# Kernel optimization log

Measured on AMD Instinct MI355X. Metric: run time of the kernel, lower is better.

Reference implementation:

```python
import jax, jax.numpy as jnp
import numpy as np

B = 16384      # batch size
L = 50         # max bag length (padded jagged)
V0, D0 = 1_000_000, 64
V1, D1 = 100_000, 128


def setup_inputs() -> dict:
    key = jax.random.key(0)
    k0, k1, k2, k3, k4, k5 = jax.random.split(key, 6)
    indices0 = jax.random.randint(k0, (B, L), 0, V0, dtype=jnp.int32)
    lengths0 = jax.random.randint(k1, (B,), 0, L + 1, dtype=jnp.int32)
    indices1 = jax.random.randint(k2, (B, L), 0, V1, dtype=jnp.int32)
    lengths1 = jax.random.randint(k3, (B,), 0, L + 1, dtype=jnp.int32)
    E0 = jax.random.normal(k4, (V0, D0), dtype=jnp.float32) * 0.01
    E1 = jax.random.normal(k5, (V1, D1), dtype=jnp.float32) * 0.01
    return {"indices0": indices0, "lengths0": lengths0,
            "indices1": indices1, "lengths1": lengths1,
            "E0": E0, "E1": E1}


def _bag_sum(E, idx, lens):
    # E: [V, D], idx: [B, L] padded indices, lens: [B] valid counts.
    # Gather rows then masked SUM-pool over the (jagged) bag dim.
    rows = E[idx]                                      # [B, L, D]
    mask = (jnp.arange(idx.shape[1])[None, :] < lens[:, None]).astype(E.dtype)  # [B, L]
    return jnp.einsum('bld,bl->bd', rows, mask)        # [B, D]


def reference(indices0, lengths0, indices1, lengths1, E0, E1):
    # EmbeddingBagCollection: per-table pooled lookup, concat along feature dim
    # (KeyedTensor layout: [B, D0 + D1]).
    p0 = _bag_sum(E0, indices0, lengths0)  # [B, 64]
    p1 = _bag_sum(E1, indices1, lengths1)  # [B, 128]
    return jnp.concatenate([p0, p1], axis=1)
```

## Files before the change

kernel.cpp:

```cpp
#include <hip/hip_runtime.h>


#define BB 16384
#define LL 50
#define D0 64
#define D1 128
#define DOUT 192

__global__ __launch_bounds__(256) void embbag_kernel(
    const int* __restrict__ idx0, const int* __restrict__ len0,
    const int* __restrict__ idx1, const int* __restrict__ len1,
    const float* __restrict__ E0, const float* __restrict__ E1,
    float* __restrict__ out)
{
    const int t    = threadIdx.x;
    const int wid  = t >> 6;
    const int lane = t & 63;
    const int b = blockIdx.x * 2 + (wid >> 1);
    const int table = wid & 1;
    if (b >= BB) return;

    if (table == 0) {
        const int sub = lane >> 4;
        const int j   = lane & 15;
        const int n   = len0[b];
        const int* __restrict__ ip = idx0 + b * LL;
        float4 acc = make_float4(0.f, 0.f, 0.f, 0.f);
        for (int base = 0; base < n; base += 4) {
            const int row = base + sub;
            if (row < n) {
                const int id = ip[row];
                const float4 v = *reinterpret_cast<const float4*>(
                    E0 + (size_t)id * D0 + j * 4);
                acc.x += v.x; acc.y += v.y; acc.z += v.z; acc.w += v.w;
            }
        }
        #pragma unroll
        for (int m = 16; m < 64; m <<= 1) {
            acc.x += __shfl_xor(acc.x, m, 64);
            acc.y += __shfl_xor(acc.y, m, 64);
            acc.z += __shfl_xor(acc.z, m, 64);
            acc.w += __shfl_xor(acc.w, m, 64);
        }
        if (sub == 0) {
            *reinterpret_cast<float4*>(out + (size_t)b * DOUT + j * 4) = acc;
        }
    } else {
        const int sub = lane >> 5;
        const int j   = lane & 31;
        const int n   = len1[b];
        const int* __restrict__ ip = idx1 + b * LL;
        float4 acc = make_float4(0.f, 0.f, 0.f, 0.f);
        for (int base = 0; base < n; base += 2) {
            const int row = base + sub;
            if (row < n) {
                const int id = ip[row];
                const float4 v = *reinterpret_cast<const float4*>(
                    E1 + (size_t)id * D1 + j * 4);
                acc.x += v.x; acc.y += v.y; acc.z += v.z; acc.w += v.w;
            }
        }
        acc.x += __shfl_xor(acc.x, 32, 64);
        acc.y += __shfl_xor(acc.y, 32, 64);
        acc.z += __shfl_xor(acc.z, 32, 64);
        acc.w += __shfl_xor(acc.w, 32, 64);
        if (sub == 0) {
            *reinterpret_cast<float4*>(out + (size_t)b * DOUT + D0 + j * 4) = acc;
        }
    }
}

extern "C" void kernel_launch(void* const* d_in, const int* in_sizes, int n_in,
                              void* d_out, int out_size, void* d_ws, size_t ws_size,
                              hipStream_t stream) {
    const int*   idx0 = (const int*)d_in[0];
    const int*   len0 = (const int*)d_in[1];
    const int*   idx1 = (const int*)d_in[2];
    const int*   len1 = (const int*)d_in[3];
    const float* E0   = (const float*)d_in[4];
    const float* E1   = (const float*)d_in[5];
    float* out = (float*)d_out;

    const int grid = BB / 2;
    embbag_kernel<<<grid, 256, 0, stream>>>(idx0, len0, idx1, len1, E0, E1, out);
}
```

Measured before the change: 60.81 us.

## Preload bag indices per wave and fully unroll gathers with masked clamped loads

Each wave now loads all 50 bag indices with one coalesced read and distributes them with shuffles, removing the dependent index load before every row gather. The loop is fully unrolled to a fixed trip count, with out-of-range rows clamped to a valid row and multiplied by zero. This lets many independent row loads be in flight at once, and two accumulators split the add chain. Empty bags exit early after writing zeros. The trade-off is redundant row reads, since padded rows fetch the last valid row again (mostly cache hits), and more registers, capped by the added occupancy hint in launch bounds.

Result: faster. 51.46 us (-15.4%).

```diff
diff --git a/kernel.cpp b/kernel.cpp
--- a/kernel.cpp
+++ b/kernel.cpp
@@ -7,7 +7,7 @@
 #define D1 128
 #define DOUT 192
 
-__global__ __launch_bounds__(256) void embbag_kernel(
+__global__ __launch_bounds__(256, 4) void embbag_kernel(
     const int* __restrict__ idx0, const int* __restrict__ len0,
     const int* __restrict__ idx1, const int* __restrict__ len1,
     const float* __restrict__ E0, const float* __restrict__ E1,
@@ -18,54 +18,83 @@
     const int lane = t & 63;
     const int b = blockIdx.x * 2 + (wid >> 1);
     const int table = wid & 1;
-    if (b >= BB) return;
 
     if (table == 0) {
+        const int n   = len0[b];
         const int sub = lane >> 4;
         const int j   = lane & 15;
-        const int n   = len0[b];
+        float* op = out + (size_t)b * DOUT + j * 4;
+        if (n == 0) {
+            if (sub == 0) *reinterpret_cast<float4*>(op) = make_float4(0.f,0.f,0.f,0.f);
+            return;
+        }
         const int* __restrict__ ip = idx0 + b * LL;
-        float4 acc = make_float4(0.f, 0.f, 0.f, 0.f);
-        for (int base = 0; base < n; base += 4) {
-            const int row = base + sub;
-            if (row < n) {
-                const int id = ip[row];
-                const float4 v = *reinterpret_cast<const float4*>(
-                    E0 + (size_t)id * D0 + j * 4);
-                acc.x += v.x; acc.y += v.y; acc.z += v.z; acc.w += v.w;
+        const int allidx = ip[lane < LL ? lane : LL - 1];
+        float4 a0 = make_float4(0.f,0.f,0.f,0.f);
+        float4 a1 = make_float4(0.f,0.f,0.f,0.f);
+        #pragma unroll
+        for (int c = 0; c < 13; ++c) {
+            const int row  = c * 4 + sub;
+            const int rowc = row < n ? row : n - 1;
+            const int id   = __shfl(allidx, rowc, 64);
+            const float s  = row < n ? 1.f : 0.f;
+            const float4 v = *reinterpret_cast<const float4*>(
+                E0 + (size_t)id * D0 + j * 4);
+            if (c & 1) {
+                a1.x = fmaf(v.x, s, a1.x); a1.y = fmaf(v.y, s, a1.y);
+                a1.z = fmaf(v.z, s, a1.z); a1.w = fmaf(v.w, s, a1.w);
+            } else {
+                a0.x = fmaf(v.x, s, a0.x); a0.y = fmaf(v.y, s, a0.y);
+                a0.z = fmaf(v.z, s, a0.z); a0.w = fmaf(v.w, s, a0.w);
             }
         }
+        a0.x += a1.x; a0.y += a1.y; a0.z += a1.z; a0.w += a1.w;
         #pragma unroll
         for (int m = 16; m < 64; m <<= 1) {
-            acc.x += __shfl_xor(acc.x, m, 64);
-            acc.y += __shfl_xor(acc.y, m, 64);
-            acc.z += __shfl_xor(acc.z, m, 64);
-            acc.w += __shfl_xor(acc.w, m, 64);
+            a0.x += __shfl_xor(a0.x, m, 64);
+            a0.y += __shfl_xor(a0.y, m, 64);
+            a0.z += __shfl_xor(a0.z, m, 64);
+            a0.w += __shfl_xor(a0.w, m, 64);
         }
         if (sub == 0) {
-            *reinterpret_cast<float4*>(out + (size_t)b * DOUT + j * 4) = acc;
+            *reinterpret_cast<float4*>(op) = a0;
         }
     } else {
+        const int n   = len1[b];
         const int sub = lane >> 5;
         const int j   = lane & 31;
-        const int n   = len1[b];
+        float* op = out + (size_t)b * DOUT + D0 + j * 4;
+        if (n == 0) {
+            if (sub == 0) *reinterpret_cast<float4*>(op) = make_float4(0.f,0.f,0.f,0.f);
+            return;
+        }
         const int* __restrict__ ip = idx1 + b * LL;
-        float4 acc = make_float4(0.f, 0.f, 0.f, 0.f);
-        for (int base = 0; base < n; base += 2) {
-            const int row = base + sub;
-            if (row < n) {
-                const int id = ip[row];
-                const float4 v = *reinterpret_cast<const float4*>(
-                    E1 + (size_t)id * D1 + j * 4);
-                acc.x += v.x; acc.y += v.y; acc.z += v.z; acc.w += v.w;
+        const int allidx = ip[lane < LL ? lane : LL - 1];
+        float4 a0 = make_float4(0.f,0.f,0.f,0.f);
+        float4 a1 = make_float4(0.f,0.f,0.f,0.f);
+        #pragma unroll
+        for (int c = 0; c < 25; ++c) {
+            const int row  = c * 2 + sub;
+            const int rowc = row < n ? row : n - 1;
+            const int id   = __shfl(allidx, rowc, 64);
+            const float s  = row < n ? 1.f : 0.f;
+            const float4 v = *reinterpret_cast<const float4*>(
+                E1 + (size_t)id * D1 + j * 4);
+            if (c & 1) {
+                a1.x = fmaf(v.x, s, a1.x); a1.y = fmaf(v.y, s, a1.y);
+                a1.z = fmaf(v.z, s, a1.z); a1.w = fmaf(v.w, s, a1.w);
+            } else {
+                a0.x = fmaf(v.x, s, a0.x); a0.y = fmaf(v.y, s, a0.y);
+                a0.z = fmaf(v.z, s, a0.z); a0.w = fmaf(v.w, s, a0.w);
             }
         }
-        acc.x += __shfl_xor(acc.x, 32, 64);
-        acc.y += __shfl_xor(acc.y, 32, 64);
-        acc.z += __shfl_xor(acc.z, 32, 64);
-        acc.w += __shfl_xor(acc.w, 32, 64);
+        a0.x += a1.x; a0.y += a1.y; a0.z += a1.z; a0.w += a1.w;
+        a0.x += __shfl_xor(a0.x, 32, 64);
+        a0.y += __shfl_xor(a0.y, 32, 64);
+        a0.z += __shfl_xor(a0.z, 32, 64);
+        a0.w += __shfl_xor(a0.w, 32, 64);
         if (sub == 0) {
-            *reinterpret_cast<float4*>(out + (size_t)b * DOUT + D0 + j * 4) = acc;
+            *reinterpret_cast<float4*>(op) = a0;
         }
     }
 }
```
